# Kernel optimization log

Measured on AMD Instinct MI355X. Metric: run time of the kernel, lower is better.

Reference implementation:

```python
import jax, jax.numpy as jnp
import numpy as np

B, T, V, E, H, K = 64, 1024, 50000, 128, 256, 20
HD = H // 2  # hidden per LSTM direction


def _p(key, i, shape, scale=0.05):
    return jax.random.normal(jax.random.fold_in(key, i), shape, dtype=jnp.float32) * scale


def setup_inputs():
    key = jax.random.key(0)
    k1, k2, k3 = jax.random.split(key, 3)
    lengths = jax.random.randint(k2, (B,), T // 4, T + 1)
    mask = jnp.arange(T)[None, :] < lengths[:, None]  # [B,T] bool, left-aligned
    x = jax.random.randint(k1, (B, T), 1, V)
    x = jnp.where(mask, x, 0).astype(jnp.int32)  # pad_idx = 0
    tags = jax.random.randint(k3, (B, T), 0, K).astype(jnp.int32)
    inp = {"x": x, "tags": tags, "mask": mask}
    pk = jax.random.key(1)
    inp["emb"] = _p(pk, 0, (V, E)).at[0].set(0.0)  # padding_idx row zeroed
    dims = [E, H]  # layer-1 input is concat of both directions = H
    i = 1
    for l in range(2):
        for suf in ["", "_rev"]:
            inp[f"w_ih_l{l}{suf}"] = _p(pk, i, (4 * HD, dims[l])); i += 1
            inp[f"w_hh_l{l}{suf}"] = _p(pk, i, (4 * HD, HD)); i += 1
            inp[f"b_ih_l{l}{suf}"] = _p(pk, i, (4 * HD,)); i += 1
            inp[f"b_hh_l{l}{suf}"] = _p(pk, i, (4 * HD,)); i += 1
    inp["ln_g"] = jnp.ones((H,), jnp.float32)
    inp["ln_b"] = jnp.zeros((H,), jnp.float32)
    inp["attn_w"] = _p(pk, i, (1, H)); i += 1
    inp["attn_b"] = _p(pk, i, (1,)); i += 1
    inp["fc1_w"] = _p(pk, i, (H, H)); i += 1
    inp["fc1_b"] = _p(pk, i, (H,)); i += 1
    inp["fc2_w"] = _p(pk, i, (K, H)); i += 1
    inp["fc2_b"] = _p(pk, i, (K,)); i += 1
    inp["crf_start"] = _p(pk, i, (K,)); i += 1
    inp["crf_end"] = _p(pk, i, (K,)); i += 1
    inp["crf_trans"] = _p(pk, i, (K, K)); i += 1
    return inp


def _lstm_dir(x, w_ih, w_hh, b_ih, b_hh, reverse):
    # x: [B,T,D] -> [B,T,HD]; torch gate order i,f,g,o
    xs = jnp.swapaxes(x, 0, 1)  # [T,B,D]
    pre = xs @ w_ih.T + b_ih + b_hh  # input contribution precomputed (GEMM)

    def step(carry, g_in):
        h, c = carry
        g = g_in + h @ w_hh.T
        i, f, gc, o = jnp.split(g, 4, axis=-1)
        c = jax.nn.sigmoid(f) * c + jax.nn.sigmoid(i) * jnp.tanh(gc)
        h = jax.nn.sigmoid(o) * jnp.tanh(c)
        return (h, c), h

    nB, nH = x.shape[0], w_hh.shape[1]
    init = (jnp.zeros((nB, nH), x.dtype), jnp.zeros((nB, nH), x.dtype))
    _, hs = jax.lax.scan(step, init, pre, reverse=reverse)
    return jnp.swapaxes(hs, 0, 1)


def _crf_nll(emissions, tags, mask, start, end, trans):
    # torchcrf: llh = score - logZ, reduction='sum'; module returns -llh.mean() (scalar)
    maskf = mask.astype(emissions.dtype)
    em_sc = jnp.take_along_axis(emissions, tags[..., None], axis=2)[..., 0]  # [B,T]
    tr_sc = trans[tags[:, :-1], tags[:, 1:]]  # [B,T-1]
    num = start[tags[:, 0]] + em_sc[:, 0] + jnp.sum(maskf[:, 1:] * (tr_sc + em_sc[:, 1:]), axis=1)
    last = jnp.sum(mask.astype(jnp.int32), axis=1) - 1
    last_tags = jnp.take_along_axis(tags, last[:, None], axis=1)[:, 0]
    num = num + end[last_tags]
    alpha0 = start[None, :] + emissions[:, 0]  # [B,K]
    em_t = jnp.swapaxes(emissions[:, 1:], 0, 1)  # [T-1,B,K]
    m_t = jnp.swapaxes(mask[:, 1:], 0, 1)  # [T-1,B]

    def step(alpha, inp):
        e, m = inp
        nxt = jax.scipy.special.logsumexp(alpha[:, :, None] + trans[None] + e[:, None, :], axis=1)
        return jnp.where(m[:, None], nxt, alpha), None

    alpha, _ = jax.lax.scan(step, alpha0, (em_t, m_t))
    logZ = jax.scipy.special.logsumexp(alpha + end[None, :], axis=1)
    return -jnp.sum(num - logZ)


def reference(x, tags, mask, emb,
              w_ih_l0, w_hh_l0, b_ih_l0, b_hh_l0,
              w_ih_l0_rev, w_hh_l0_rev, b_ih_l0_rev, b_hh_l0_rev,
              w_ih_l1, w_hh_l1, b_ih_l1, b_hh_l1,
              w_ih_l1_rev, w_hh_l1_rev, b_ih_l1_rev, b_hh_l1_rev,
              ln_g, ln_b, attn_w, attn_b, fc1_w, fc1_b, fc2_w, fc2_b,
              crf_start, crf_end, crf_trans):
    mask = mask.at[:, 0].set(True)
    h = emb[x]  # [B,T,E]
    # 2-layer bidirectional LSTM (eval mode: dropout = identity)
    h = jnp.concatenate([
        _lstm_dir(h, w_ih_l0, w_hh_l0, b_ih_l0, b_hh_l0, False),
        _lstm_dir(h, w_ih_l0_rev, w_hh_l0_rev, b_ih_l0_rev, b_hh_l0_rev, True)], axis=-1)
    h = jnp.concatenate([
        _lstm_dir(h, w_ih_l1, w_hh_l1, b_ih_l1, b_hh_l1, False),
        _lstm_dir(h, w_ih_l1_rev, w_hh_l1_rev, b_ih_l1_rev, b_hh_l1_rev, True)], axis=-1)
    # LayerNorm (eps=1e-5)
    mu = jnp.mean(h, axis=-1, keepdims=True)
    var = jnp.mean(jnp.square(h - mu), axis=-1, keepdims=True)
    h = (h - mu) * jax.lax.rsqrt(var + 1e-5) * ln_g + ln_b
    # masked attention + residual broadcast of context
    scores = (h @ attn_w.T)[..., 0] + attn_b[0]  # [B,T]
    scores = jnp.where(mask, scores, jnp.float32(-1e9))
    w = jax.nn.softmax(scores, axis=1)[..., None]  # [B,T,1]
    h = h + jnp.sum(h * w, axis=1, keepdims=True)
    # hidden_fc: Linear + ReLU (dropout identity in eval)
    h = jax.nn.relu(h @ fc1_w.T + fc1_b)
    emissions = h @ fc2_w.T + fc2_b  # [B,T,K]
    return _crf_nll(emissions, tags, mask, crf_start, crf_end, crf_trans)
```

## Files before the change

### kernel.cpp

```cpp
#include <hip/hip_runtime.h>
#include <stdint.h>

#define BB 64
#define TT 1024
#define EE 128

typedef __bf16 bf16x8 __attribute__((ext_vector_type(8)));
typedef float f32x4 __attribute__((ext_vector_type(4)));

#define MFMA16 __builtin_amdgcn_mfma_f32_16x16x32_bf16

__device__ __forceinline__ float bf2f(unsigned short u) {
  union { unsigned int i; float f; } v; v.i = ((unsigned int)u) << 16; return v.f;
}
__device__ __forceinline__ unsigned short f2bf(float f) {
  union { float f; unsigned int i; } v; v.f = f;
  return (unsigned short)((v.i + 0x7fffu + ((v.i >> 16) & 1u)) >> 16);
}
__device__ __forceinline__ float sigf(float x) {
  return __builtin_amdgcn_rcpf(1.f + __expf(-x));
}
__device__ __forceinline__ float tanhf_(float x) {
  return fmaf(2.f, __builtin_amdgcn_rcpf(1.f + __expf(-2.f * x)), -1.f);
}


__global__ __launch_bounds__(256) void cvt_all(const float* s0, unsigned short* d0,
                                               const float* s1, unsigned short* d1,
                                               const float* s2, unsigned short* d2,
                                               const float* s3, unsigned short* d3,
                                               const float* s4, unsigned short* d4,
                                               const float* s5, unsigned short* d5,
                                               const float* s6, unsigned short* d6,
                                               const float* s7, unsigned short* d7,
                                               const float* s8, unsigned short* d8) {
  int i = blockIdx.x * 256 + threadIdx.x;
  const float* s; unsigned short* d; int off;
  if      (i <  16384) { s = s0; d = d0; off = 0; }
  else if (i <  32768) { s = s1; d = d1; off = 16384; }
  else if (i <  65536) { s = s2; d = d2; off = 32768; }
  else if (i <  98304) { s = s3; d = d3; off = 65536; }
  else if (i < 114688) { s = s4; d = d4; off = 98304; }
  else if (i < 131072) { s = s5; d = d5; off = 114688; }
  else if (i < 147456) { s = s6; d = d6; off = 131072; }
  else if (i < 163840) { s = s7; d = d7; off = 147456; }
  else                 { s = s8; d = d8; off = 163840; }
  int k = i - off;
  float4 v = *(const float4*)&s[(size_t)k * 4];
  ushort4 o; o.x = f2bf(v.x); o.y = f2bf(v.y); o.z = f2bf(v.z); o.w = f2bf(v.w);
  *(ushort4*)&d[(size_t)k * 4] = o;
}

__global__ __launch_bounds__(256) void bias_comb(const float* bi, const float* bh,
                                                 const float* bir, const float* bhr,
                                                 float* __restrict__ o) {
  int j = blockIdx.x * 256 + threadIdx.x;
  if (j < 1024) o[j] = (j < 512) ? (bi[j] + bh[j]) : (bir[j - 512] + bhr[j - 512]);
}

__global__ __launch_bounds__(256) void embed_k(const int* __restrict__ x,
                                               const float* __restrict__ emb,
                                               unsigned short* __restrict__ xe) {
  int i = blockIdx.x * 256 + threadIdx.x;
  int bt = i >> 5, e4 = (i & 31) << 2;
  float4 v = *(const float4*)&emb[(size_t)x[bt] * EE + e4];
  ushort4 o; o.x = f2bf(v.x); o.y = f2bf(v.y); o.z = f2bf(v.z); o.w = f2bf(v.w);
  *(ushort4*)&xe[(size_t)bt * EE + e4] = o;
}


template <bool RELU, bool REMAP>
__global__ __launch_bounds__(256) void gemm128(const unsigned short* __restrict__ A,
                                               const unsigned short* __restrict__ W,
                                               const float* __restrict__ bias,
                                               unsigned short* __restrict__ out,
                                               int M, int N, int K) {
  __shared__ unsigned short LB[2 * 128 * 72];
  const int tid = threadIdx.x, wave = tid >> 6, lane = tid & 63;
  const int fr = lane & 15, q = lane >> 4;
  const int m0 = blockIdx.x * 128, n0 = blockIdx.y * 128;
  const int wm = (wave & 1) * 64, wn = (wave >> 1) * 64;
  f32x4 acc[4][4] = {};
  const int sr = tid >> 1, sc = (tid & 1) * 32;

  for (int k0 = 0; k0 < K; k0 += 64) {
    const unsigned short* ga = &A[(size_t)(m0 + sr) * K + k0 + sc];
    const unsigned short* gw = &W[(size_t)(n0 + sr) * K + k0 + sc];
    uint4 a0 = *(const uint4*)&ga[0],  a1 = *(const uint4*)&ga[8];
    uint4 a2 = *(const uint4*)&ga[16], a3 = *(const uint4*)&ga[24];
    uint4 w0 = *(const uint4*)&gw[0],  w1 = *(const uint4*)&gw[8];
    uint4 w2 = *(const uint4*)&gw[16], w3 = *(const uint4*)&gw[24];
    __syncthreads();
    *(uint4*)&LB[sr * 72 + sc +  0] = a0;
    *(uint4*)&LB[sr * 72 + sc +  8] = a1;
    *(uint4*)&LB[sr * 72 + sc + 16] = a2;
    *(uint4*)&LB[sr * 72 + sc + 24] = a3;
    *(uint4*)&LB[9216 + sr * 72 + sc +  0] = w0;
    *(uint4*)&LB[9216 + sr * 72 + sc +  8] = w1;
    *(uint4*)&LB[9216 + sr * 72 + sc + 16] = w2;
    *(uint4*)&LB[9216 + sr * 72 + sc + 24] = w3;
    __syncthreads();
#pragma unroll
    for (int kt = 0; kt < 2; kt++) {
      bf16x8 afr[4], bfr[4];
#pragma unroll
      for (int i = 0; i < 4; i++)
        afr[i] = *(const bf16x8*)&LB[(wm + i * 16 + fr) * 72 + kt * 32 + q * 8];
#pragma unroll
      for (int j = 0; j < 4; j++)
        bfr[j] = *(const bf16x8*)&LB[9216 + (wn + j * 16 + fr) * 72 + kt * 32 + q * 8];
#pragma unroll
      for (int i = 0; i < 4; i++)
#pragma unroll
        for (int j = 0; j < 4; j++)
          acc[i][j] = MFMA16(afr[i], bfr[j], acc[i][j], 0, 0, 0);
    }
  }
  __syncthreads();
  const int cc = fr, cr = q * 4;
#pragma unroll
  for (int j = 0; j < 4; j++) {
    float bs = bias[n0 + wn + j * 16 + cc];
#pragma unroll
    for (int i = 0; i < 4; i++)
#pragma unroll
      for (int rr = 0; rr < 4; rr++) {
        float v = acc[i][j][rr] + bs;
        if (RELU) v = fmaxf(v, 0.f);
        LB[(wm + i * 16 + cr + rr) * 136 + wn + j * 16 + cc] = f2bf(v);
      }
  }
  __syncthreads();
  const int row = tid >> 1, hf = (tid & 1) * 64;
  const int gm = m0 + row;
  size_t off;
  if (REMAP) { int b = gm >> 10, t = gm & 1023; off = ((size_t)(t * 64 + b)) * N + n0 + hf; }
  else       { off = (size_t)gm * N + n0 + hf; }
#pragma unroll
  for (int j = 0; j < 8; j++) {
    uint4 v = *(const uint4*)&LB[row * 136 + hf + j * 8];
    *(uint4*)&out[off + j * 8] = v;
  }
}


#define SCAN_STEP10(PG0, PG1, PG2, PG3, TIDX) {                               \
    bf16x8 bv0 = *(const bf16x8*)&hS[p][q * 8];                               \
    bf16x8 bv1 = *(const bf16x8*)&hS[p][32 + q * 8];                          \
    bf16x8 bv2 = *(const bf16x8*)&hS[p][64 + q * 8];                          \
    bf16x8 bv3 = *(const bf16x8*)&hS[p][96 + q * 8];                          \
    f32x4 c0 = {0,0,0,0}, c1 = {0,0,0,0}, c2 = {0,0,0,0}, c3 = {0,0,0,0};     \
    c0 = MFMA16(bv0, af[0][0], c0, 0,0,0); c1 = MFMA16(bv0, af[1][0], c1, 0,0,0); \
    c2 = MFMA16(bv0, af[2][0], c2, 0,0,0); c3 = MFMA16(bv0, af[3][0], c3, 0,0,0); \
    c0 = MFMA16(bv1, af[0][1], c0, 0,0,0); c1 = MFMA16(bv1, af[1][1], c1, 0,0,0); \
    c2 = MFMA16(bv1, af[2][1], c2, 0,0,0); c3 = MFMA16(bv1, af[3][1], c3, 0,0,0); \
    c0 = MFMA16(bv2, af[0][2], c0, 0,0,0); c1 = MFMA16(bv2, af[1][2], c1, 0,0,0); \
    c2 = MFMA16(bv2, af[2][2], c2, 0,0,0); c3 = MFMA16(bv2, af[3][2], c3, 0,0,0); \
    c0 = MFMA16(bv3, af[0][3], c0, 0,0,0); c1 = MFMA16(bv3, af[1][3], c1, 0,0,0); \
    c2 = MFMA16(bv3, af[2][3], c2, 0,0,0); c3 = MFMA16(bv3, af[3][3], c3, 0,0,0); \
    float gi = c0[0] + bf2f(PG0);                                             \
    float gf = c1[0] + bf2f(PG1);                                             \
    float gg = c2[0] + bf2f(PG2);                                             \
    float go = c3[0] + bf2f(PG3);                                             \
    float cn = sigf(gf) * c + sigf(gi) * tanhf_(gg);                          \
    c = cn;                                                                   \
    float h = sigf(go) * tanhf_(cn);                                          \
    unsigned short hb_ = f2bf(h);                                             \
    if (q == 0) {                                                             \
      hS[p ^ 1][u] = hb_;                                                     \
      hob[(size_t)(TIDX) * 256] = hb_;                   \
    }                                                                         \
  }

__global__ __launch_bounds__(512) void lstm_scan10(const unsigned short* __restrict__ pre,
                                                   const unsigned short* __restrict__ whhb,
                                                   unsigned short* __restrict__ hout) {
  const int b = blockIdx.x, dir = blockIdx.y;
  const int tid = threadIdx.x;
  const int w = tid >> 6, lane = tid & 63;
  const int fr = lane & 15, q = lane >> 4;
  const int u = 16 * w + fr;
  const unsigned short* wb = whhb + (size_t)dir * 65536;

  bf16x8 af[4][4];
#pragma unroll
  for (int G = 0; G < 4; G++)
#pragma unroll
    for (int kt = 0; kt < 4; kt++)
      af[G][kt] = *(const bf16x8*)&wb[(size_t)(128 * G + 16 * w + fr) * 128 + kt * 32 + q * 8];
  asm volatile("" : "+v"(af[0][0]), "+v"(af[0][1]), "+v"(af[0][2]), "+v"(af[0][3]),
                    "+v"(af[1][0]), "+v"(af[1][1]), "+v"(af[1][2]), "+v"(af[1][3]),
                    "+v"(af[2][0]), "+v"(af[2][1]), "+v"(af[2][2]), "+v"(af[2][3]),
                    "+v"(af[3][0]), "+v"(af[3][1]), "+v"(af[3][2]), "+v"(af[3][3]));

  __shared__ alignas(16) unsigned short hS[2][128];
  if (tid < 128) { hS[0][tid] = 0; hS[1][tid] = 0; }

  const int t0 = dir ? 1023 : 0, st = dir ? -1 : 1;
  float c = 0.f;
  const unsigned short* pb = pre + (size_t)b * 1024 + dir * 512 + u;
  unsigned short* hob = hout + (size_t)b * 1024 * 256 + dir * 128 + u;

  unsigned short pA0, pA1, pA2, pA3, pB0, pB1, pB2, pB3;
  {
    size_t tb = (size_t)t0 * 65536;
    pA0 = pb[tb]; pA1 = pb[tb + 128]; pA2 = pb[tb + 256]; pA3 = pb[tb + 384];
    tb = (size_t)(t0 + st) * 65536;
    pB0 = pb[tb]; pB1 = pb[tb + 128]; pB2 = pb[tb + 256]; pB3 = pb[tb + 384];
  }
  __syncthreads();

  int p = 0;
  for (int s = 0; s < 1024; s += 2) {
    const int t = t0 + st * s;
    SCAN_STEP10(pA0, pA1, pA2, pA3, t)
    if (s + 2 < 1024) {
      size_t tb = (size_t)(t0 + st * (s + 2)) * 65536;
      pA0 = pb[tb]; pA1 = pb[tb + 128]; pA2 = pb[tb + 256]; pA3 = pb[tb + 384];
    }
    asm volatile("s_waitcnt lgkmcnt(0)\n\ts_barrier" ::: "memory");
    p ^= 1;
    SCAN_STEP10(pB0, pB1, pB2, pB3, t + st)
    if (s + 3 < 1024) {
      size_t tb = (size_t)(t0 + st * (s + 3)) * 65536;
      pB0 = pb[tb]; pB1 = pb[tb + 128]; pB2 = pb[tb + 256]; pB3 = pb[tb + 384];
    }
    asm volatile("s_waitcnt lgkmcnt(0)\n\ts_barrier" ::: "memory");
    p ^= 1;
  }
}


__global__ __launch_bounds__(256) void ln_attn(const unsigned short* __restrict__ h,
                                               const float* __restrict__ g,
                                               const float* __restrict__ be,
                                               const float* __restrict__ aw,
                                               const float* __restrict__ ab,
                                               unsigned short* __restrict__ hln,
                                               float* __restrict__ sc) {
  int row = blockIdx.x * 4 + (threadIdx.x >> 6);
  int lane = threadIdx.x & 63;
  ushort4 u = *(const ushort4*)&h[(size_t)row * 256 + lane * 4];
  float vx = bf2f(u.x), vy = bf2f(u.y), vz = bf2f(u.z), vw = bf2f(u.w);
  float s = vx + vy + vz + vw;
#pragma unroll
  for (int o = 1; o < 64; o <<= 1) s += __shfl_xor(s, o);
  float mu = s * (1.f / 256.f);
  float dx = vx - mu, dy = vy - mu, dz = vz - mu, dw = vw - mu;
  float q = dx * dx + dy * dy + dz * dz + dw * dw;
#pragma unroll
  for (int o = 1; o < 64; o <<= 1) q += __shfl_xor(q, o);
  float inv = rsqrtf(q * (1.f / 256.f) + 1e-5f);
  float4 gg = *(const float4*)&g[lane * 4];
  float4 bb = *(const float4*)&be[lane * 4];
  float y0 = dx * inv * gg.x + bb.x;
  float y1 = dy * inv * gg.y + bb.y;
  float y2 = dz * inv * gg.z + bb.z;
  float y3 = dw * inv * gg.w + bb.w;
  ushort4 ov; ov.x = f2bf(y0); ov.y = f2bf(y1); ov.z = f2bf(y2); ov.w = f2bf(y3);
  *(ushort4*)&hln[(size_t)row * 256 + lane * 4] = ov;
  float4 av = *(const float4*)&aw[lane * 4];
  float p = y0 * av.x + y1 * av.y + y2 * av.z + y3 * av.w;
#pragma unroll
  for (int o = 1; o < 64; o <<= 1) p += __shfl_xor(p, o);
  if (lane == 0) sc[row] = p + ab[0];
}


__global__ __launch_bounds__(256) void attn_pool_h2(const float* __restrict__ scores,
                                                    const int* __restrict__ x,
                                                    const unsigned short* __restrict__ h_ln,
                                                    unsigned short* __restrict__ h2) {
  int b = blockIdx.x, tid = threadIdx.x;
  __shared__ float wls[1024];
  __shared__ float red[4];
  float mx = -1e30f;
  for (int t = tid; t < 1024; t += 256) {
    bool valid = (t == 0) || (x[b * 1024 + t] != 0);
    float s = valid ? scores[b * 1024 + t] : -1e9f;
    wls[t] = s;
    mx = fmaxf(mx, s);
  }
#pragma unroll
  for (int o = 1; o < 64; o <<= 1) mx = fmaxf(mx, __shfl_xor(mx, o));
  if ((tid & 63) == 0) red[tid >> 6] = mx;
  __syncthreads();
  mx = fmaxf(fmaxf(red[0], red[1]), fmaxf(red[2], red[3]));
  __syncthreads();
  float sm = 0.f;
  for (int t = tid; t < 1024; t += 256) {
    float e = __expf(wls[t] - mx);
    wls[t] = e;
    sm += e;
  }
#pragma unroll
  for (int o = 1; o < 64; o <<= 1) sm += __shfl_xor(sm, o);
  if ((tid & 63) == 0) red[tid >> 6] = sm;
  __syncthreads();
  sm = red[0] + red[1] + red[2] + red[3];
  float inv = 1.f / sm;
  float a0 = 0.f, a1 = 0.f, a2 = 0.f, a3 = 0.f;
  const unsigned short* hb = h_ln + (size_t)b * 1024 * 256 + tid;
  for (int t = 0; t < 1024; t += 4) {
    a0 = fmaf(wls[t + 0], bf2f(hb[(size_t)(t + 0) * 256]), a0);
    a1 = fmaf(wls[t + 1], bf2f(hb[(size_t)(t + 1) * 256]), a1);
    a2 = fmaf(wls[t + 2], bf2f(hb[(size_t)(t + 2) * 256]), a2);
    a3 = fmaf(wls[t + 3], bf2f(hb[(size_t)(t + 3) * 256]), a3);
  }
  float pooled = ((a0 + a1) + (a2 + a3)) * inv;
  unsigned short* ob = h2 + (size_t)b * 1024 * 256 + tid;
#pragma unroll 4
  for (int t = 0; t < 1024; t++)
    ob[(size_t)t * 256] = f2bf(bf2f(hb[(size_t)t * 256]) + pooled);
}


__global__ __launch_bounds__(256) void fc2_emis(const unsigned short* __restrict__ fin,
                                                const float* __restrict__ w,
                                                const float* __restrict__ bias,
                                                float* __restrict__ em) {
  int row = blockIdx.x * 4 + (threadIdx.x >> 6);
  int lane = threadIdx.x & 63;
  ushort4 u = *(const ushort4*)&fin[(size_t)row * 256 + lane * 4];
  float x0 = bf2f(u.x), x1 = bf2f(u.y), x2 = bf2f(u.z), x3 = bf2f(u.w);
  float acc[20];
#pragma unroll
  for (int jj = 0; jj < 20; jj++) {
    float4 wv = *(const float4*)&w[jj * 256 + lane * 4];
    acc[jj] = x0 * wv.x + x1 * wv.y + x2 * wv.z + x3 * wv.w;
  }
#pragma unroll
  for (int jj = 0; jj < 20; jj++) {
#pragma unroll
    for (int o = 1; o < 64; o <<= 1) acc[jj] += __shfl_xor(acc[jj], o);
  }
  if (lane == 0) {
#pragma unroll
    for (int jj = 0; jj < 20; jj++) em[(size_t)row * 20 + jj] = acc[jj] + bias[jj];
  }
}


__global__ __launch_bounds__(64) void crf_k(const float* __restrict__ em,
                                            const int* __restrict__ tags,
                                            const int* __restrict__ x,
                                            const float* __restrict__ cs,
                                            const float* __restrict__ ce,
                                            const float* __restrict__ ctr,
                                            float* __restrict__ part) {
  int b = blockIdx.x, lane = threadIdx.x;
  const float* eb = em + (size_t)b * 1024 * 20;
  const int* tb = tags + b * 1024;
  const int* xb = x + b * 1024;

  int cnt = 0;
  for (int t = lane; t < 1024; t += 64) cnt += (t == 0 || xb[t] != 0) ? 1 : 0;
#pragma unroll
  for (int o = 1; o < 64; o <<= 1) cnt += __shfl_xor(cnt, o);
  int len = cnt;

  float ns = 0.f;
  for (int t = 1 + lane; t < len; t += 64)
    ns += ctr[tb[t - 1] * 20 + tb[t]] + eb[(size_t)t * 20 + tb[t]];
#pragma unroll
  for (int o = 1; o < 64; o <<= 1) ns += __shfl_xor(ns, o);
  float num = ns + cs[tb[0]] + eb[tb[0]] + ce[tb[len - 1]];

  __shared__ float al[32];
  if (lane < 32) al[lane] = (lane < 20) ? (cs[lane] + eb[lane]) : -1e30f;
  __syncthreads();

  int p = lane / 20, jj = lane % 20;
  int i0 = p * 7;
  float trc[7];
#pragma unroll
  for (int i = 0; i < 7; i++)
    trc[i] = (i0 + i < 20) ? ctr[(i0 + i) * 20 + jj] : -1e30f;

  for (int t = 1; t < len; t++) {
    float aa[7];
    float m = -3e30f;
#pragma unroll
    for (int i = 0; i < 7; i++) {
      float a = ((i0 + i < 28) ? al[i0 + i] : -1e30f) + trc[i];
      aa[i] = a;
      m = fmaxf(m, a);
    }
    float m0 = __shfl(m, jj), m1 = __shfl(m, jj + 20), m2 = __shfl(m, jj + 40);
    float mj = fmaxf(fmaxf(m0, m1), m2);
    float s = 0.f;
#pragma unroll
    for (int i = 0; i < 7; i++) s += __expf(aa[i] - mj);
    float s0 = __shfl(s, jj), s1 = __shfl(s, jj + 20), s2 = __shfl(s, jj + 40);
    float na = mj + __logf(s0 + s1 + s2) + eb[(size_t)t * 20 + jj];
    __syncthreads();
    if (lane < 20) al[lane] = na;
    __syncthreads();
  }

  float v = (lane < 20) ? (al[lane] + ce[lane]) : -3e30f;
  float mm = v;
#pragma unroll
  for (int o = 1; o < 64; o <<= 1) mm = fmaxf(mm, __shfl_xor(mm, o));
  float ss = (lane < 20) ? __expf(v - mm) : 0.f;
#pragma unroll
  for (int o = 1; o < 64; o <<= 1) ss += __shfl_xor(ss, o);
  float logZ = mm + __logf(ss);
  if (lane == 0) part[b] = logZ - num;
}

__global__ __launch_bounds__(64) void finalsum(const float* __restrict__ part,
                                               float* __restrict__ out) {
  float v = part[threadIdx.x];
#pragma unroll
  for (int o = 1; o < 64; o <<= 1) v += __shfl_xor(v, o);
  if (threadIdx.x == 0) out[0] = v;
}


extern "C" void kernel_launch(void* const* d_in, const int* in_sizes, int n_in,
                              void* d_out, int out_size, void* d_ws, size_t ws_size,
                              hipStream_t stream) {
  (void)in_sizes; (void)n_in; (void)out_size; (void)ws_size;
  const int*   x     = (const int*)  d_in[0];
  const int*   tags  = (const int*)  d_in[1];
  const float* emb   = (const float*)d_in[3];
  const float* wih0  = (const float*)d_in[4];
  const float* whh0  = (const float*)d_in[5];
  const float* bih0  = (const float*)d_in[6];
  const float* bhh0  = (const float*)d_in[7];
  const float* wih0r = (const float*)d_in[8];
  const float* whh0r = (const float*)d_in[9];
  const float* bih0r = (const float*)d_in[10];
  const float* bhh0r = (const float*)d_in[11];
  const float* wih1  = (const float*)d_in[12];
  const float* whh1  = (const float*)d_in[13];
  const float* bih1  = (const float*)d_in[14];
  const float* bhh1  = (const float*)d_in[15];
  const float* wih1r = (const float*)d_in[16];
  const float* whh1r = (const float*)d_in[17];
  const float* bih1r = (const float*)d_in[18];
  const float* bhh1r = (const float*)d_in[19];
  const float* lng   = (const float*)d_in[20];
  const float* lnb   = (const float*)d_in[21];
  const float* attw  = (const float*)d_in[22];
  const float* attb  = (const float*)d_in[23];
  const float* fc1w  = (const float*)d_in[24];
  const float* fc1b  = (const float*)d_in[25];
  const float* fc2w  = (const float*)d_in[26];
  const float* fc2b  = (const float*)d_in[27];
  const float* cst   = (const float*)d_in[28];
  const float* cen   = (const float*)d_in[29];
  const float* ctr   = (const float*)d_in[30];

  char* base = (char*)d_ws;
  const size_t MB = 1024 * 1024;

  unsigned short* PRE  = (unsigned short*)(base);
  unsigned short* HLN  = (unsigned short*)(base);
  unsigned short* H2   = (unsigned short*)(base + 64 * MB);
  unsigned short* FC1O = (unsigned short*)(base + 96 * MB);
  unsigned short* XEMB = (unsigned short*)(base + 128 * MB);
  unsigned short* HL0  = (unsigned short*)(base + 128 * MB);
  unsigned short* HL1  = (unsigned short*)(base + 128 * MB);
  float*          EM   = (float*)(base + 128 * MB);
  char* sm = base + 160 * MB;
  unsigned short* WIH0  = (unsigned short*)sm;  sm += (size_t)2 * 512 * 128 * 2;
  unsigned short* WIH1  = (unsigned short*)sm;  sm += (size_t)2 * 512 * 256 * 2;
  unsigned short* FC1W  = (unsigned short*)sm;  sm += (size_t)256 * 256 * 2;
  unsigned short* WHHB0 = (unsigned short*)sm;  sm += (size_t)2 * 512 * 128 * 2;
  unsigned short* WHHB1 = (unsigned short*)sm;  sm += (size_t)2 * 512 * 128 * 2;
  float* BIAS0 = (float*)sm; sm += 1024 * 4;
  float* BIAS1 = (float*)sm; sm += 1024 * 4;
  float* SCORE = (float*)sm; sm += (size_t)BB * TT * 4;
  float* PART  = (float*)sm; sm += 256;

  cvt_all<<<704, 256, 0, stream>>>(wih0, WIH0,
                                   wih0r, WIH0 + 65536,
                                   wih1, WIH1,
                                   wih1r, WIH1 + 131072,
                                   fc1w, FC1W,
                                   whh0, WHHB0,
                                   whh0r, WHHB0 + 65536,
                                   whh1, WHHB1,
                                   whh1r, WHHB1 + 65536);
  bias_comb<<<4, 256, 0, stream>>>(bih0, bhh0, bih0r, bhh0r, BIAS0);
  bias_comb<<<4, 256, 0, stream>>>(bih1, bhh1, bih1r, bhh1r, BIAS1);

  embed_k<<<8192, 256, 0, stream>>>(x, emb, XEMB);

  gemm128<false, true><<<dim3(512, 8), 256, 0, stream>>>(XEMB, WIH0, BIAS0, PRE, 65536, 1024, 128);
  lstm_scan10<<<dim3(64, 2), 512, 0, stream>>>(PRE, WHHB0, HL0);

  gemm128<false, true><<<dim3(512, 8), 256, 0, stream>>>(HL0, WIH1, BIAS1, PRE, 65536, 1024, 256);
  lstm_scan10<<<dim3(64, 2), 512, 0, stream>>>(PRE, WHHB1, HL1);

  ln_attn<<<16384, 256, 0, stream>>>(HL1, lng, lnb, attw, attb, HLN, SCORE);
  attn_pool_h2<<<64, 256, 0, stream>>>(SCORE, x, HLN, H2);

  gemm128<true, false><<<dim3(512, 2), 256, 0, stream>>>(H2, FC1W, fc1b, FC1O, 65536, 256, 256);
  fc2_emis<<<16384, 256, 0, stream>>>(FC1O, fc2w, fc2b, EM);

  crf_k<<<64, 64, 0, stream>>>(EM, tags, x, cst, cen, ctr, PART);
  finalsum<<<1, 64, 0, stream>>>(PART, (float*)d_out);
}
```

Baseline: 1.733 ms.

## Fuse LSTM input projection into scan kernel and split attention residual add

Removes the separate input-projection GEMMs. Each LSTM scan block now computes its gate pre-activations with MFMA for chunks of 16 timesteps into shared memory, interleaved with the recurrence. This avoids writing and re-reading the large PRE buffer. The cost is extra compute and global weight loads inside the latency-bound scan, which only uses 128 blocks. Separately, the serial per-batch residual broadcast is split out of the attention-pool kernel into a wide elementwise h2add kernel, and workspace buffers are reassigned.

```diff
diff --git a/kernel.cpp b/kernel.cpp
--- a/kernel.cpp
+++ b/kernel.cpp
@@ -69,7 +69,7 @@
 }
 
 
-template <bool RELU, bool REMAP>
+template <bool RELU>
 __global__ __launch_bounds__(256) void gemm128(const unsigned short* __restrict__ A,
                                                const unsigned short* __restrict__ W,
                                                const float* __restrict__ bias,
@@ -132,10 +132,7 @@
   }
   __syncthreads();
   const int row = tid >> 1, hf = (tid & 1) * 64;
-  const int gm = m0 + row;
-  size_t off;
-  if (REMAP) { int b = gm >> 10, t = gm & 1023; off = ((size_t)(t * 64 + b)) * N + n0 + hf; }
-  else       { off = (size_t)gm * N + n0 + hf; }
+  size_t off = (size_t)(m0 + row) * N + n0 + hf;
 #pragma unroll
   for (int j = 0; j < 8; j++) {
     uint4 v = *(const uint4*)&LB[row * 136 + hf + j * 8];
@@ -144,7 +141,7 @@
 }
 
 
-#define SCAN_STEP10(PG0, PG1, PG2, PG3, TIDX) {                               \
+#define SCAN_STEP11(PG0, PG1, PG2, PG3, TIDX) {                               \
     bf16x8 bv0 = *(const bf16x8*)&hS[p][q * 8];                               \
     bf16x8 bv1 = *(const bf16x8*)&hS[p][32 + q * 8];                          \
     bf16x8 bv2 = *(const bf16x8*)&hS[p][64 + q * 8];                          \
@@ -172,15 +169,21 @@
     }                                                                         \
   }
 
-__global__ __launch_bounds__(512) void lstm_scan10(const unsigned short* __restrict__ pre,
-                                                   const unsigned short* __restrict__ whhb,
-                                                   unsigned short* __restrict__ hout) {
+template <int KT>
+__global__ __launch_bounds__(512) void lstm_scan11(
+    const unsigned short* __restrict__ xin,
+    const unsigned short* __restrict__ wih,
+    const unsigned short* __restrict__ whhb,
+    const float* __restrict__ bias,
+    unsigned short* __restrict__ hout) {
+  const int K = KT * 32;
   const int b = blockIdx.x, dir = blockIdx.y;
   const int tid = threadIdx.x;
   const int w = tid >> 6, lane = tid & 63;
   const int fr = lane & 15, q = lane >> 4;
   const int u = 16 * w + fr;
   const unsigned short* wb = whhb + (size_t)dir * 65536;
+  const unsigned short* wi = wih + (size_t)dir * 512 * K;
 
   bf16x8 af[4][4];
 #pragma unroll
@@ -193,40 +196,56 @@
                     "+v"(af[2][0]), "+v"(af[2][1]), "+v"(af[2][2]), "+v"(af[2][3]),
                     "+v"(af[3][0]), "+v"(af[3][1]), "+v"(af[3][2]), "+v"(af[3][3]));
 
+  float bs0 = bias[dir * 512 +   0 + u];
+  float bs1 = bias[dir * 512 + 128 + u];
+  float bs2 = bias[dir * 512 + 256 + u];
+  float bs3 = bias[dir * 512 + 384 + u];
+
   __shared__ alignas(16) unsigned short hS[2][128];
+  __shared__ alignas(16) unsigned short preS[16][512];
   if (tid < 128) { hS[0][tid] = 0; hS[1][tid] = 0; }
 
   const int t0 = dir ? 1023 : 0, st = dir ? -1 : 1;
   float c = 0.f;
-  const unsigned short* pb = pre + (size_t)b * 1024 + dir * 512 + u;
+  const unsigned short* xb = xin + (size_t)b * 1024 * K;
   unsigned short* hob = hout + (size_t)b * 1024 * 256 + dir * 128 + u;
 
-  unsigned short pA0, pA1, pA2, pA3, pB0, pB1, pB2, pB3;
-  {
-    size_t tb = (size_t)t0 * 65536;
-    pA0 = pb[tb]; pA1 = pb[tb + 128]; pA2 = pb[tb + 256]; pA3 = pb[tb + 384];
-    tb = (size_t)(t0 + st) * 65536;
-    pB0 = pb[tb]; pB1 = pb[tb + 128]; pB2 = pb[tb + 256]; pB3 = pb[tb + 384];
-  }
   __syncthreads();
 
   int p = 0;
-  for (int s = 0; s < 1024; s += 2) {
-    const int t = t0 + st * s;
-    SCAN_STEP10(pA0, pA1, pA2, pA3, t)
-    if (s + 2 < 1024) {
-      size_t tb = (size_t)(t0 + st * (s + 2)) * 65536;
-      pA0 = pb[tb]; pA1 = pb[tb + 128]; pA2 = pb[tb + 256]; pA3 = pb[tb + 384];
+  for (int j = 0; j < 64; j++) {
+    {
+      const int tfr = t0 + st * (16 * j + fr);
+      bf16x8 xf[KT];
+#pragma unroll
+      for (int kt = 0; kt < KT; kt++)
+        xf[kt] = *(const bf16x8*)&xb[(size_t)tfr * K + kt * 32 + q * 8];
+      float bsv[4] = {bs0, bs1, bs2, bs3};
+#pragma unroll
+      for (int g = 0; g < 4; g++) {
+        f32x4 acc = {0, 0, 0, 0};
+#pragma unroll
+        for (int kt = 0; kt < KT; kt++) {
+          bf16x8 wf = *(const bf16x8*)&wi[(size_t)(g * 128 + 16 * w + fr) * K + kt * 32 + q * 8];
+          acc = MFMA16(xf[kt], wf, acc, 0, 0, 0);
+        }
+#pragma unroll
+        for (int r = 0; r < 4; r++)
+          preS[4 * q + r][g * 128 + u] = f2bf(acc[r] + bsv[g]);
+      }
     }
     asm volatile("s_waitcnt lgkmcnt(0)\n\ts_barrier" ::: "memory");
-    p ^= 1;
-    SCAN_STEP10(pB0, pB1, pB2, pB3, t + st)
-    if (s + 3 < 1024) {
-      size_t tb = (size_t)(t0 + st * (s + 3)) * 65536;
-      pB0 = pb[tb]; pB1 = pb[tb + 128]; pB2 = pb[tb + 256]; pB3 = pb[tb + 384];
+#pragma unroll 2
+    for (int s16 = 0; s16 < 16; s16++) {
+      const int t = t0 + st * (16 * j + s16);
+      unsigned short pg0 = preS[s16][u];
+      unsigned short pg1 = preS[s16][128 + u];
+      unsigned short pg2 = preS[s16][256 + u];
+      unsigned short pg3 = preS[s16][384 + u];
+      SCAN_STEP11(pg0, pg1, pg2, pg3, t)
+      asm volatile("s_waitcnt lgkmcnt(0)\n\ts_barrier" ::: "memory");
+      p ^= 1;
     }
-    asm volatile("s_waitcnt lgkmcnt(0)\n\ts_barrier" ::: "memory");
-    p ^= 1;
   }
 }
 
@@ -267,10 +286,10 @@
 }
 
 
-__global__ __launch_bounds__(256) void attn_pool_h2(const float* __restrict__ scores,
-                                                    const int* __restrict__ x,
-                                                    const unsigned short* __restrict__ h_ln,
-                                                    unsigned short* __restrict__ h2) {
+__global__ __launch_bounds__(256) void attn_pool(const float* __restrict__ scores,
+                                                 const int* __restrict__ x,
+                                                 const unsigned short* __restrict__ h_ln,
+                                                 float* __restrict__ pooled) {
   int b = blockIdx.x, tid = threadIdx.x;
   __shared__ float wls[1024];
   __shared__ float red[4];
@@ -307,11 +326,21 @@
     a2 = fmaf(wls[t + 2], bf2f(hb[(size_t)(t + 2) * 256]), a2);
     a3 = fmaf(wls[t + 3], bf2f(hb[(size_t)(t + 3) * 256]), a3);
   }
-  float pooled = ((a0 + a1) + (a2 + a3)) * inv;
-  unsigned short* ob = h2 + (size_t)b * 1024 * 256 + tid;
-#pragma unroll 4
-  for (int t = 0; t < 1024; t++)
-    ob[(size_t)t * 256] = f2bf(bf2f(hb[(size_t)t * 256]) + pooled);
+  pooled[b * 256 + tid] = ((a0 + a1) + (a2 + a3)) * inv;
+}
+
+__global__ __launch_bounds__(256) void h2add(const unsigned short* __restrict__ h_ln,
+                                             const float* __restrict__ pooled,
+                                             unsigned short* __restrict__ h2) {
+  size_t i = ((size_t)blockIdx.x * 256 + threadIdx.x) * 4;
+  int b = (int)(i >> 18);
+  int cidx = (int)(i & 255);
+  ushort4 v = *(const ushort4*)&h_ln[i];
+  float4 p = *(const float4*)&pooled[b * 256 + cidx];
+  ushort4 o;
+  o.x = f2bf(bf2f(v.x) + p.x); o.y = f2bf(bf2f(v.y) + p.y);
+  o.z = f2bf(bf2f(v.z) + p.z); o.w = f2bf(bf2f(v.w) + p.w);
+  *(ushort4*)&h2[i] = o;
 }
 
 
@@ -456,14 +485,13 @@
   char* base = (char*)d_ws;
   const size_t MB = 1024 * 1024;
 
-  unsigned short* PRE  = (unsigned short*)(base);
-  unsigned short* HLN  = (unsigned short*)(base);
-  unsigned short* H2   = (unsigned short*)(base + 64 * MB);
-  unsigned short* FC1O = (unsigned short*)(base + 96 * MB);
+  unsigned short* HL0  = (unsigned short*)(base);
+  unsigned short* HL1  = (unsigned short*)(base + 32 * MB);
+  unsigned short* HLN  = (unsigned short*)(base + 64 * MB);
+  float*          EM   = (float*)(base + 64 * MB);
+  unsigned short* H2   = (unsigned short*)(base + 96 * MB);
   unsigned short* XEMB = (unsigned short*)(base + 128 * MB);
-  unsigned short* HL0  = (unsigned short*)(base + 128 * MB);
-  unsigned short* HL1  = (unsigned short*)(base + 128 * MB);
-  float*          EM   = (float*)(base + 128 * MB);
+  unsigned short* FC1O = (unsigned short*)(base + 128 * MB);
   char* sm = base + 160 * MB;
   unsigned short* WIH0  = (unsigned short*)sm;  sm += (size_t)2 * 512 * 128 * 2;
   unsigned short* WIH1  = (unsigned short*)sm;  sm += (size_t)2 * 512 * 256 * 2;
@@ -473,6 +501,7 @@
   float* BIAS0 = (float*)sm; sm += 1024 * 4;
   float* BIAS1 = (float*)sm; sm += 1024 * 4;
   float* SCORE = (float*)sm; sm += (size_t)BB * TT * 4;
+  float* POOL  = (float*)sm; sm += 64 * 256 * 4;
   float* PART  = (float*)sm; sm += 256;
 
   cvt_all<<<704, 256, 0, stream>>>(wih0, WIH0,
@@ -489,16 +518,14 @@
 
   embed_k<<<8192, 256, 0, stream>>>(x, emb, XEMB);
 
-  gemm128<false, true><<<dim3(512, 8), 256, 0, stream>>>(XEMB, WIH0, BIAS0, PRE, 65536, 1024, 128);
-  lstm_scan10<<<dim3(64, 2), 512, 0, stream>>>(PRE, WHHB0, HL0);
-
-  gemm128<false, true><<<dim3(512, 8), 256, 0, stream>>>(HL0, WIH1, BIAS1, PRE, 65536, 1024, 256);
-  lstm_scan10<<<dim3(64, 2), 512, 0, stream>>>(PRE, WHHB1, HL1);
+  lstm_scan11<4><<<dim3(64, 2), 512, 0, stream>>>(XEMB, WIH0, WHHB0, BIAS0, HL0);
+  lstm_scan11<8><<<dim3(64, 2), 512, 0, stream>>>(HL0, WIH1, WHHB1, BIAS1, HL1);
 
   ln_attn<<<16384, 256, 0, stream>>>(HL1, lng, lnb, attw, attb, HLN, SCORE);
-  attn_pool_h2<<<64, 256, 0, stream>>>(SCORE, x, HLN, H2);
-
-  gemm128<true, false><<<dim3(512, 2), 256, 0, stream>>>(H2, FC1W, fc1b, FC1O, 65536, 256, 256);
+  attn_pool<<<64, 256, 0, stream>>>(SCORE, x, HLN, POOL);
+  h2add<<<16384, 256, 0, stream>>>(HLN, POOL, H2);
+
+  gemm128<true><<<dim3(512, 2), 256, 0, stream>>>(H2, FC1W, fc1b, FC1O, 65536, 256, 256);
   fc2_emis<<<16384, 256, 0, stream>>>(FC1O, fc2w, fc2b, EM);
 
   crf_k<<<64, 64, 0, stream>>>(EM, tags, x, cst, cen, ctr, PART);
```

New measurement: 1.756 ms. Within noise of the previous version (+1.3%).

## Split attention pooling into parallel reduction and separate broadcast-add kernel

Applied to the files above, without the earlier changes.

The single 64-block attention-pool kernel, which both reduced over time and wrote the residual output, is split in two. The first kernel computes pooled context over a 64x4 grid, with each block's four wavefronts reducing interleaved time steps for 64 channels. The second is a fully parallel elementwise kernel that adds the pooled vector to h_ln using vectorized loads and stores. The aim is to remove the low-occupancy serial write loop, which ran on only 64 blocks. The cost is an extra launch, a small pooled buffer, and softmax recomputed in each of the four y-blocks.

```diff
diff --git a/kernel.cpp b/kernel.cpp
--- a/kernel.cpp
+++ b/kernel.cpp
@@ -267,11 +267,11 @@
 }
 
 
-__global__ __launch_bounds__(256) void attn_pool_h2(const float* __restrict__ scores,
-                                                    const int* __restrict__ x,
-                                                    const unsigned short* __restrict__ h_ln,
-                                                    unsigned short* __restrict__ h2) {
-  int b = blockIdx.x, tid = threadIdx.x;
+__global__ __launch_bounds__(256) void attn_pool(const float* __restrict__ scores,
+                                                 const int* __restrict__ x,
+                                                 const unsigned short* __restrict__ h_ln,
+                                                 float* __restrict__ pooled) {
+  int b = blockIdx.x, cq = blockIdx.y, tid = threadIdx.x;
   __shared__ float wls[1024];
   __shared__ float red[4];
   float mx = -1e30f;
@@ -299,19 +299,32 @@
   __syncthreads();
   sm = red[0] + red[1] + red[2] + red[3];
   float inv = 1.f / sm;
-  float a0 = 0.f, a1 = 0.f, a2 = 0.f, a3 = 0.f;
-  const unsigned short* hb = h_ln + (size_t)b * 1024 * 256 + tid;
-  for (int t = 0; t < 1024; t += 4) {
-    a0 = fmaf(wls[t + 0], bf2f(hb[(size_t)(t + 0) * 256]), a0);
-    a1 = fmaf(wls[t + 1], bf2f(hb[(size_t)(t + 1) * 256]), a1);
-    a2 = fmaf(wls[t + 2], bf2f(hb[(size_t)(t + 2) * 256]), a2);
-    a3 = fmaf(wls[t + 3], bf2f(hb[(size_t)(t + 3) * 256]), a3);
-  }
-  float pooled = ((a0 + a1) + (a2 + a3)) * inv;
-  unsigned short* ob = h2 + (size_t)b * 1024 * 256 + tid;
-#pragma unroll 4
-  for (int t = 0; t < 1024; t++)
-    ob[(size_t)t * 256] = f2bf(bf2f(hb[(size_t)t * 256]) + pooled);
+  int ch = cq * 64 + (tid & 63), ph = tid >> 6;
+  float a = 0.f;
+  const unsigned short* hb = h_ln + (size_t)b * 1024 * 256 + ch;
+  for (int t = ph; t < 1024; t += 4)
+    a = fmaf(wls[t], bf2f(hb[(size_t)t * 256]), a);
+  __syncthreads();
+  wls[ph * 64 + (tid & 63)] = a;
+  __syncthreads();
+  if (tid < 64) {
+    float v = (wls[tid] + wls[64 + tid]) + (wls[128 + tid] + wls[192 + tid]);
+    pooled[b * 256 + ch] = v * inv;
+  }
+}
+
+__global__ __launch_bounds__(256) void h2add(const unsigned short* __restrict__ h_ln,
+                                             const float* __restrict__ pooled,
+                                             unsigned short* __restrict__ h2) {
+  size_t i = ((size_t)blockIdx.x * 256 + threadIdx.x) * 4;
+  int b = (int)(i >> 18);
+  int cidx = (int)(i & 255);
+  ushort4 v = *(const ushort4*)&h_ln[i];
+  float4 p = *(const float4*)&pooled[b * 256 + cidx];
+  ushort4 o;
+  o.x = f2bf(bf2f(v.x) + p.x); o.y = f2bf(bf2f(v.y) + p.y);
+  o.z = f2bf(bf2f(v.z) + p.z); o.w = f2bf(bf2f(v.w) + p.w);
+  *(ushort4*)&h2[i] = o;
 }
 
 
@@ -473,6 +486,7 @@
   float* BIAS0 = (float*)sm; sm += 1024 * 4;
   float* BIAS1 = (float*)sm; sm += 1024 * 4;
   float* SCORE = (float*)sm; sm += (size_t)BB * TT * 4;
+  float* POOL  = (float*)sm; sm += 64 * 256 * 4;
   float* PART  = (float*)sm; sm += 256;
 
   cvt_all<<<704, 256, 0, stream>>>(wih0, WIH0,
@@ -496,7 +510,8 @@
   lstm_scan10<<<dim3(64, 2), 512, 0, stream>>>(PRE, WHHB1, HL1);
 
   ln_attn<<<16384, 256, 0, stream>>>(HL1, lng, lnb, attw, attb, HLN, SCORE);
-  attn_pool_h2<<<64, 256, 0, stream>>>(SCORE, x, HLN, H2);
+  attn_pool<<<dim3(64, 4), 256, 0, stream>>>(SCORE, x, HLN, POOL);
+  h2add<<<16384, 256, 0, stream>>>(HLN, POOL, H2);
 
   gemm128<true, false><<<dim3(512, 2), 256, 0, stream>>>(H2, FC1W, fc1b, FC1O, 65536, 256, 256);
   fc2_emis<<<16384, 256, 0, stream>>>(FC1O, fc2w, fc2b, EM);
```

Measured after the change: 1.743 ms. No clear change (+0.6%).
